# Optimization experiments

Measured on AMD Instinct MI355X. Metric: run time of the kernel, lower is better.

The kernel has to match this reference:

```python
import jax, jax.numpy as jnp
import numpy as np

N_NODES = 100000   # number of graph nodes
N_EDGES = 1000000  # number of edges
D_IN = 64          # input feature dim
D_OUT = 64         # output feature dim
N_RELS = 16        # number of relation types


def setup_inputs() -> dict:
    key = jax.random.key(0)
    k1, k2, k3, k4, k5 = jax.random.split(key, 5)
    feat = jax.random.normal(k1, (N_NODES, D_IN), dtype=jnp.float32)
    weight = jax.random.normal(k2, (N_RELS, D_IN, D_OUT), dtype=jnp.float32) * 0.05
    src = jax.random.randint(k3, (N_EDGES,), 0, N_NODES)
    dst = jax.random.randint(k4, (N_EDGES,), 0, N_NODES)
    etypes = jax.random.randint(k5, (N_EDGES,), 0, N_RELS)
    return {"feat": feat, "weight": weight, "src": src, "dst": dst, "etypes": etypes}


def reference(feat, weight, src, dst, etypes):
    # gather source-node features per edge: h = edges.src['h']
    h = feat[src]                                # [E, d_in]
    n_rels = weight.shape[0]
    e, d_out = h.shape[0], weight.shape[2]

    # gather_mm(h, weight, idx_b=etypes): m_e = h_e @ weight[etypes_e]
    # grouped-GEMM realized as R masked dense GEMMs (R is small, fixed);
    # avoids materializing the [E, d_in, d_out] gathered weight tensor.
    def step(m, rw):
        r, w_r = rw
        mask = jnp.where(etypes == r, 1.0, 0.0).astype(h.dtype)  # [E]
        m = m + mask[:, None] * (h @ w_r)                        # [E, d_out]
        return m, None

    m0 = jnp.zeros((e, d_out), dtype=h.dtype)
    m, _ = jax.lax.scan(step, m0, (jnp.arange(n_rels), weight))

    # update_all(..., fn.sum('m', 'h')): scatter-sum messages to dst nodes
    out = jax.ops.segment_sum(m, dst, num_segments=feat.shape[0])  # [N, d_out]
    return out
```

## Files before the change

### kernel.cpp

```cpp
#include <hip/hip_runtime.h>
#include <hip/hip_bf16.h>
#include <stdint.h>

#define NNODES 100000
#define NEDGES 1000000
#define DIM 64
#define NRELS 16
#define EPB 2048
#define NB ((NEDGES + EPB - 1) / EPB)
#define PADCAP (NEDGES + NRELS * 64)
#define MAXTILES (PADCAP / 64)
#define NDN NNODES
#define DCH 1024
#define NCHUNK ((NDN + DCH - 1) / DCH)

#define WS_NEED 151805824ull

using short8  = __attribute__((ext_vector_type(8))) short;
using floatx4 = __attribute__((ext_vector_type(4))) float;

__device__ __forceinline__ unsigned short f2bf(float f) {
    union { float f; uint32_t u; } v; v.f = f;
    uint32_t u = v.u;
    return (unsigned short)((u + 0x7FFFu + ((u >> 16) & 1u)) >> 16);
}
__device__ __forceinline__ float bf2f(uint32_t u16) {
    union { uint32_t u; float f; } v; v.u = u16 << 16;
    return v.f;
}
__device__ __forceinline__ uint32_t pk2(float a, float b) {
    __hip_bfloat162 h = __float22bfloat162_rn(make_float2(a, b));
    union { __hip_bfloat162 h; uint32_t u; } v; v.h = h;
    return v.u;
}

__global__ void k_convert_feat(const float* __restrict__ feat,
                               unsigned short* __restrict__ featB) {
    int i = (blockIdx.x * blockDim.x + threadIdx.x) * 4;
    const float4 f = *(const float4*)(feat + i);
    ushort4 o;
    o.x = f2bf(f.x); o.y = f2bf(f.y); o.z = f2bf(f.z); o.w = f2bf(f.w);
    *(ushort4*)(featB + i) = o;
}

__global__ void k_convert_w(const float* __restrict__ W,
                            unsigned short* __restrict__ Wt) {
    int t = blockIdx.x * blockDim.x + threadIdx.x;
    int r = t >> 12, n = (t >> 6) & 63, k = t & 63;
    Wt[t] = f2bf(W[(r << 12) + (k << 6) + n]);
}

__global__ void k_hist(const int* __restrict__ et, const int* __restrict__ dst,
                       int* __restrict__ hist, int* __restrict__ dhist,
                       unsigned short* __restrict__ rank) {
    __shared__ int cnt[16];
    if (threadIdx.x < 16) cnt[threadIdx.x] = 0;
    __syncthreads();
    int start = blockIdx.x * EPB;
    int end = min(NEDGES, start + EPB);
    for (int i = start + threadIdx.x; i < end; i += 256) {
        atomicAdd(&cnt[et[i]], 1);
        rank[i] = (unsigned short)atomicAdd(&dhist[dst[i]], 1);
    }
    __syncthreads();
    if (threadIdx.x < 16) hist[blockIdx.x * 16 + threadIdx.x] = cnt[threadIdx.x];
}

__global__ void k_scan(const int* __restrict__ hist, int* __restrict__ bbase,
                       int* __restrict__ Pve) {
    __shared__ int s_cnt[16];
    __shared__ int s_P[17];
    int w = threadIdx.x >> 6;
    int lane = threadIdx.x & 63;
    int carry = 0;
    for (int c = 0; c < NB; c += 64) {
        int idx = c + lane;
        int v = (idx < NB) ? hist[idx * 16 + w] : 0;
        int x = v;
        #pragma unroll
        for (int off = 1; off < 64; off <<= 1) {
            int y = __shfl_up(x, off);
            if (lane >= off) x += y;
        }
        if (idx < NB) bbase[idx * 16 + w] = carry + x - v;
        carry += __shfl(x, 63);
    }
    if (lane == 0) s_cnt[w] = carry;
    __syncthreads();
    if (threadIdx.x == 0) {
        int p = 0;
        for (int r = 0; r < 16; ++r) {
            s_P[r] = p;
            Pve[r] = p;
            Pve[17 + r] = p + s_cnt[r];
            p += (s_cnt[r] + 63) & ~63;
        }
        s_P[16] = p;
        Pve[16] = p;
    }
    __syncthreads();
    int pw = s_P[w];
    for (int idx = lane; idx < NB; idx += 64)
        bbase[idx * 16 + w] += pw;
}

__global__ void k_dscanA(const int* __restrict__ dhist, int* __restrict__ dbase,
                         int* __restrict__ csum) {
    __shared__ int wsum[16];
    __shared__ int woff[16];
    int t = threadIdx.x;
    int i = blockIdx.x * DCH + t;
    int v = (i < NDN) ? dhist[i] : 0;
    int lane = t & 63, wv = t >> 6;
    int x = v;
    #pragma unroll
    for (int off = 1; off < 64; off <<= 1) {
        int y = __shfl_up(x, off);
        if (lane >= off) x += y;
    }
    if (lane == 63) wsum[wv] = x;
    __syncthreads();
    if (wv == 0) {
        int s = (lane < 16) ? wsum[lane] : 0;
        #pragma unroll
        for (int off = 1; off < 16; off <<= 1) {
            int y = __shfl_up(s, off);
            if (lane >= off) s += y;
        }
        if (lane < 16) woff[lane] = s - wsum[lane];
        if (lane == 15) csum[blockIdx.x] = s;
    }
    __syncthreads();
    if (i < NDN) dbase[i] = woff[wv] + x - v;
}

__global__ void k_dscanB(int* __restrict__ dbase, const int* __restrict__ csum) {
    __shared__ int soff;
    int b = blockIdx.x, t = threadIdx.x;
    if (t < 64) {
        int s = ((t < b) ? csum[t] : 0) + ((t + 64 < b) ? csum[t + 64] : 0);
        #pragma unroll
        for (int off = 32; off >= 1; off >>= 1) s += __shfl_down(s, off);
        if (t == 0) soff = s;
    }
    __syncthreads();
    int i = b * DCH + t;
    if (i < NDN) dbase[i] += soff;
}

__global__ void k_scatter(const int* __restrict__ et, const int* __restrict__ src,
                          const int* __restrict__ dst, const int* __restrict__ bbase,
                          const int* __restrict__ dbase,
                          const unsigned short* __restrict__ rank,
                          int2* __restrict__ pairS, int buildPos) {
    __shared__ int base[16];
    if (threadIdx.x < 16) base[threadIdx.x] = bbase[blockIdx.x * 16 + threadIdx.x];
    __syncthreads();
    int start = blockIdx.x * EPB;
    int end = min(NEDGES, start + EPB);
    for (int i = start + threadIdx.x; i < end; i += 256) {
        int r = et[i];
        int pos = atomicAdd(&base[r], 1);
        int d = dst[i];
        int second = buildPos ? (dbase[d] + (int)rank[i]) : d;
        pairS[pos] = make_int2(src[i], second);
    }
}

__global__ void __launch_bounds__(256)
k_computeA(const unsigned short* __restrict__ featB,
           const unsigned short* __restrict__ Wt,
           const int2* __restrict__ pairS, const int* __restrict__ Pve,
           unsigned short* __restrict__ msgE) {
    __shared__ float lds[4][16 * 68];
    const int w = threadIdx.x >> 6;
    const int t = blockIdx.x * 4 + w;
    const int base = t * 64;
    const int total = Pve[16];
    if (base >= total) return;
    int r = 0;
    while (base >= Pve[r + 1]) ++r;
    const int validEnd = Pve[17 + r];
    const int lane = threadIdx.x & 63;
    const int quad = lane >> 4;
    const int l16 = lane & 15;

    const unsigned short* wr = Wt + (r << 12);
    short8 bfr[4][2];
    #pragma unroll
    for (int tn = 0; tn < 4; ++tn)
        #pragma unroll
        for (int ks = 0; ks < 2; ++ks)
            bfr[tn][ks] = *(const short8*)(wr + ((tn * 16 + l16) << 6) + ks * 32 + quad * 8);

    const int rr = lane >> 2, seg = lane & 3;
    #pragma unroll
    for (int tm = 0; tm < 4; ++tm) {
        int row = base + tm * 16 + l16;
        int s = (row < validEnd) ? pairS[row].x : 0;
        const unsigned short* fp = featB + (s << 6) + quad * 8;
        short8 a0 = *(const short8*)(fp);
        short8 a1 = *(const short8*)(fp + 32);
        #pragma unroll
        for (int tn = 0; tn < 4; ++tn) {
            floatx4 c = {0.f, 0.f, 0.f, 0.f};
            c = __builtin_amdgcn_mfma_f32_16x16x32_bf16(a0, bfr[tn][0], c, 0, 0, 0);
            c = __builtin_amdgcn_mfma_f32_16x16x32_bf16(a1, bfr[tn][1], c, 0, 0, 0);
            #pragma unroll
            for (int j = 0; j < 4; ++j)
                lds[w][(quad * 4 + j) * 68 + tn * 16 + l16] = c[j];
        }
        int rowi = base + tm * 16 + rr;
        int p = (rowi < validEnd) ? pairS[rowi].y : -1;
        if (p >= 0) {
            const float* lp = &lds[w][rr * 68 + seg * 16];
            uint4 o0, o1;
            o0.x = pk2(lp[0],  lp[1]);  o0.y = pk2(lp[2],  lp[3]);
            o0.z = pk2(lp[4],  lp[5]);  o0.w = pk2(lp[6],  lp[7]);
            o1.x = pk2(lp[8],  lp[9]);  o1.y = pk2(lp[10], lp[11]);
            o1.z = pk2(lp[12], lp[13]); o1.w = pk2(lp[14], lp[15]);
            uint32_t* op = (uint32_t*)(msgE + (size_t)p * 64 + seg * 16);
            *(uint4*)(op)     = o0;
            *(uint4*)(op + 4) = o1;
        }
    }
}

__global__ void __launch_bounds__(256)
k_reduce(const unsigned short* __restrict__ msgE,
         const int* __restrict__ dbase, float* __restrict__ out) {
    int n = blockIdx.x * 4 + (threadIdx.x >> 6);
    if (n >= NDN) return;
    int lane = threadIdx.x & 63;
    int start = dbase[n];
    int end = (n + 1 < NDN) ? dbase[n + 1] : NEDGES;
    int c4 = (lane & 15) * 4;
    float ax = 0.f, ay = 0.f, az = 0.f, aw = 0.f;
    for (int row = start + (lane >> 4); row < end; row += 4) {
        uint2 v = *(const uint2*)(msgE + (size_t)row * 64 + c4);
        ax += bf2f(v.x & 0xffffu); ay += bf2f(v.x >> 16);
        az += bf2f(v.y & 0xffffu); aw += bf2f(v.y >> 16);
    }
    ax += __shfl_xor(ax, 16); ax += __shfl_xor(ax, 32);
    ay += __shfl_xor(ay, 16); ay += __shfl_xor(ay, 32);
    az += __shfl_xor(az, 16); az += __shfl_xor(az, 32);
    aw += __shfl_xor(aw, 16); aw += __shfl_xor(aw, 32);
    if (lane < 16) {
        float4 o = make_float4(ax, ay, az, aw);
        *(float4*)(out + (size_t)n * 64 + lane * 4) = o;
    }
}

__global__ void __launch_bounds__(256)
k_compute(const unsigned short* __restrict__ featB,
          const unsigned short* __restrict__ Wt,
          const int2* __restrict__ pairS, const int* __restrict__ Pve,
          float* __restrict__ out) {
    const int t = blockIdx.x * 4 + (threadIdx.x >> 6);
    const int base = t * 64;
    const int total = Pve[16];
    if (base >= total) return;
    int r = 0;
    while (base >= Pve[r + 1]) ++r;
    const int validEnd = Pve[17 + r];
    const int lane = threadIdx.x & 63;
    const int quad = lane >> 4;
    const int l16 = lane & 15;

    const unsigned short* wr = Wt + (r << 12);
    short8 bfr[4][2];
    #pragma unroll
    for (int tn = 0; tn < 4; ++tn)
        #pragma unroll
        for (int ks = 0; ks < 2; ++ks)
            bfr[tn][ks] = *(const short8*)(wr + ((tn * 16 + l16) << 6) + ks * 32 + quad * 8);

    #pragma unroll
    for (int tm = 0; tm < 4; ++tm) {
        int row = base + tm * 16 + l16;
        int s = (row < validEnd) ? pairS[row].x : 0;
        const unsigned short* fp = featB + (s << 6) + quad * 8;
        short8 a0 = *(const short8*)(fp);
        short8 a1 = *(const short8*)(fp + 32);
        floatx4 cc[4];
        #pragma unroll
        for (int tn = 0; tn < 4; ++tn) {
            floatx4 c = {0.f, 0.f, 0.f, 0.f};
            c = __builtin_amdgcn_mfma_f32_16x16x32_bf16(a0, bfr[tn][0], c, 0, 0, 0);
            c = __builtin_amdgcn_mfma_f32_16x16x32_bf16(a1, bfr[tn][1], c, 0, 0, 0);
            cc[tn] = c;
        }
        int pos0 = base + tm * 16 + quad * 4;
        #pragma unroll
        for (int j = 0; j < 4; ++j) {
            if (pos0 + j < validEnd) {
                int dn = pairS[pos0 + j].y;
                float* op = out + (dn << 6) + l16;
                #pragma unroll
                for (int tn = 0; tn < 4; ++tn)
                    atomicAdd(op + tn * 16, cc[tn][j]);
            }
        }
    }
}

extern "C" void kernel_launch(void* const* d_in, const int* in_sizes, int n_in,
                              void* d_out, int out_size, void* d_ws, size_t ws_size,
                              hipStream_t stream) {
    const float* feat = (const float*)d_in[0];
    const float* W    = (const float*)d_in[1];
    const int* src    = (const int*)d_in[2];
    const int* dst    = (const int*)d_in[3];
    const int* et     = (const int*)d_in[4];
    float* out = (float*)d_out;
    char* ws = (char*)d_ws;

    unsigned short* featB = (unsigned short*)(ws);
    unsigned short* Wt    = (unsigned short*)(ws + 12800000);
    int* hist  = (int*)(ws + 12931072);
    int* bbase = (int*)(ws + 12963840);
    int* Pve   = (int*)(ws + 12996608);
    int* dhist = (int*)(ws + 12996864);
    int* dbase = (int*)(ws + 13396992);
    int* csum  = (int*)(ws + 13797120);
    unsigned short* rank = (unsigned short*)(ws + 13797632);
    int2* pairS = (int2*)(ws + 15797632);
    unsigned short* msgE = (unsigned short*)(ws + 23805824);

    const int usePhases = (ws_size >= WS_NEED) ? 1 : 0;

    k_convert_feat<<<6250, 256, 0, stream>>>(feat, featB);
    k_convert_w<<<256, 256, 0, stream>>>(W, Wt);
    hipMemsetAsync(dhist, 0, NDN * sizeof(int), stream);
    k_hist<<<NB, 256, 0, stream>>>(et, dst, hist, dhist, rank);
    k_scan<<<1, 1024, 0, stream>>>(hist, bbase, Pve);

    if (usePhases) {
        k_dscanA<<<NCHUNK, DCH, 0, stream>>>(dhist, dbase, csum);
        k_dscanB<<<NCHUNK, DCH, 0, stream>>>(dbase, csum);
        k_scatter<<<NB, 256, 0, stream>>>(et, src, dst, bbase, dbase, rank, pairS, 1);
        k_computeA<<<(MAXTILES + 3) / 4, 256, 0, stream>>>(featB, Wt, pairS, Pve, msgE);
        k_reduce<<<(NDN + 3) / 4, 256, 0, stream>>>(msgE, dbase, out);
    } else {
        hipMemsetAsync(d_out, 0, (size_t)out_size * sizeof(float), stream);
        k_scatter<<<NB, 256, 0, stream>>>(et, src, dst, bbase, dbase, rank, pairS, 0);
        k_compute<<<(MAXTILES + 3) / 4, 256, 0, stream>>>(featB, Wt, pairS, Pve, out);
    }
}
```

Before: 244.5 us.

## Fuse setup kernels, use nontemporal message stores, widen reduce loads

Merges the feature conversion, weight transpose/convert and histogram kernels into one launch that dispatches by block index, removing two kernel launches and their serialization gaps. The per-edge message writes in the compute kernel and the reads in the reduce kernel switch to nontemporal builtins to reduce cache pollution from the streaming bf16 message buffer. The reduce kernel now has each lane load 16 bytes (8 bf16) and processes 8 rows per wavefront iteration instead of 4, with an extra shuffle stage. Nontemporal hints may hurt if the message buffer would otherwise hit in L2 between compute and reduce.

```diff
diff --git a/kernel.cpp b/kernel.cpp
--- a/kernel.cpp
+++ b/kernel.cpp
@@ -14,10 +14,15 @@
 #define DCH 1024
 #define NCHUNK ((NDN + DCH - 1) / DCH)
 
+#define FEAT_BLKS 6250
+#define W_BLKS 256
+#define SETUP_BLKS (FEAT_BLKS + W_BLKS + NB)
+
 #define WS_NEED 151805824ull
 
 using short8  = __attribute__((ext_vector_type(8))) short;
 using floatx4 = __attribute__((ext_vector_type(4))) float;
+using uintx4  = __attribute__((ext_vector_type(4))) unsigned int;
 
 __device__ __forceinline__ unsigned short f2bf(float f) {
     union { float f; uint32_t u; } v; v.f = f;
@@ -34,36 +39,36 @@
     return v.u;
 }
 
-__global__ void k_convert_feat(const float* __restrict__ feat,
-                               unsigned short* __restrict__ featB) {
-    int i = (blockIdx.x * blockDim.x + threadIdx.x) * 4;
-    const float4 f = *(const float4*)(feat + i);
-    ushort4 o;
-    o.x = f2bf(f.x); o.y = f2bf(f.y); o.z = f2bf(f.z); o.w = f2bf(f.w);
-    *(ushort4*)(featB + i) = o;
-}
-
-__global__ void k_convert_w(const float* __restrict__ W,
-                            unsigned short* __restrict__ Wt) {
-    int t = blockIdx.x * blockDim.x + threadIdx.x;
-    int r = t >> 12, n = (t >> 6) & 63, k = t & 63;
-    Wt[t] = f2bf(W[(r << 12) + (k << 6) + n]);
-}
-
-__global__ void k_hist(const int* __restrict__ et, const int* __restrict__ dst,
-                       int* __restrict__ hist, int* __restrict__ dhist,
-                       unsigned short* __restrict__ rank) {
+__global__ void k_setup(const float* __restrict__ feat, const float* __restrict__ W,
+                        const int* __restrict__ et, const int* __restrict__ dst,
+                        unsigned short* __restrict__ featB, unsigned short* __restrict__ Wt,
+                        int* __restrict__ hist, int* __restrict__ dhist,
+                        unsigned short* __restrict__ rank) {
     __shared__ int cnt[16];
-    if (threadIdx.x < 16) cnt[threadIdx.x] = 0;
-    __syncthreads();
-    int start = blockIdx.x * EPB;
-    int end = min(NEDGES, start + EPB);
-    for (int i = start + threadIdx.x; i < end; i += 256) {
-        atomicAdd(&cnt[et[i]], 1);
-        rank[i] = (unsigned short)atomicAdd(&dhist[dst[i]], 1);
-    }
-    __syncthreads();
-    if (threadIdx.x < 16) hist[blockIdx.x * 16 + threadIdx.x] = cnt[threadIdx.x];
+    const int b = blockIdx.x;
+    if (b < FEAT_BLKS) {
+        int i = (b * 256 + threadIdx.x) * 4;
+        const float4 f = *(const float4*)(feat + i);
+        ushort4 o;
+        o.x = f2bf(f.x); o.y = f2bf(f.y); o.z = f2bf(f.z); o.w = f2bf(f.w);
+        *(ushort4*)(featB + i) = o;
+    } else if (b < FEAT_BLKS + W_BLKS) {
+        int t = (b - FEAT_BLKS) * 256 + threadIdx.x;
+        int r = t >> 12, n = (t >> 6) & 63, k = t & 63;
+        Wt[t] = f2bf(W[(r << 12) + (k << 6) + n]);
+    } else {
+        const int bb = b - (FEAT_BLKS + W_BLKS);
+        if (threadIdx.x < 16) cnt[threadIdx.x] = 0;
+        __syncthreads();
+        int start = bb * EPB;
+        int end = min(NEDGES, start + EPB);
+        for (int i = start + threadIdx.x; i < end; i += 256) {
+            atomicAdd(&cnt[et[i]], 1);
+            rank[i] = (unsigned short)atomicAdd(&dhist[dst[i]], 1);
+        }
+        __syncthreads();
+        if (threadIdx.x < 16) hist[bb * 16 + threadIdx.x] = cnt[threadIdx.x];
+    }
 }
 
 __global__ void k_scan(const int* __restrict__ hist, int* __restrict__ bbase,
@@ -214,14 +219,14 @@
         int p = (rowi < validEnd) ? pairS[rowi].y : -1;
         if (p >= 0) {
             const float* lp = &lds[w][rr * 68 + seg * 16];
-            uint4 o0, o1;
+            uintx4 o0, o1;
             o0.x = pk2(lp[0],  lp[1]);  o0.y = pk2(lp[2],  lp[3]);
             o0.z = pk2(lp[4],  lp[5]);  o0.w = pk2(lp[6],  lp[7]);
             o1.x = pk2(lp[8],  lp[9]);  o1.y = pk2(lp[10], lp[11]);
             o1.z = pk2(lp[12], lp[13]); o1.w = pk2(lp[14], lp[15]);
-            uint32_t* op = (uint32_t*)(msgE + (size_t)p * 64 + seg * 16);
-            *(uint4*)(op)     = o0;
-            *(uint4*)(op + 4) = o1;
+            uintx4* op = (uintx4*)(msgE + (size_t)p * 64 + seg * 16);
+            __builtin_nontemporal_store(o0, op);
+            __builtin_nontemporal_store(o1, op + 1);
         }
     }
 }
@@ -234,20 +239,28 @@
     int lane = threadIdx.x & 63;
     int start = dbase[n];
     int end = (n + 1 < NDN) ? dbase[n + 1] : NEDGES;
-    int c4 = (lane & 15) * 4;
-    float ax = 0.f, ay = 0.f, az = 0.f, aw = 0.f;
-    for (int row = start + (lane >> 4); row < end; row += 4) {
-        uint2 v = *(const uint2*)(msgE + (size_t)row * 64 + c4);
-        ax += bf2f(v.x & 0xffffu); ay += bf2f(v.x >> 16);
-        az += bf2f(v.y & 0xffffu); aw += bf2f(v.y >> 16);
-    }
-    ax += __shfl_xor(ax, 16); ax += __shfl_xor(ax, 32);
-    ay += __shfl_xor(ay, 16); ay += __shfl_xor(ay, 32);
-    az += __shfl_xor(az, 16); az += __shfl_xor(az, 32);
-    aw += __shfl_xor(aw, 16); aw += __shfl_xor(aw, 32);
-    if (lane < 16) {
-        float4 o = make_float4(ax, ay, az, aw);
-        *(float4*)(out + (size_t)n * 64 + lane * 4) = o;
+    int c8 = (lane & 7) * 8;
+    float a0 = 0.f, a1 = 0.f, a2 = 0.f, a3 = 0.f;
+    float a4 = 0.f, a5 = 0.f, a6 = 0.f, a7 = 0.f;
+    for (int row = start + (lane >> 3); row < end; row += 8) {
+        const uintx4* p = (const uintx4*)(msgE + (size_t)row * 64 + c8);
+        uintx4 v = __builtin_nontemporal_load(p);
+        a0 += bf2f(v.x & 0xffffu); a1 += bf2f(v.x >> 16);
+        a2 += bf2f(v.y & 0xffffu); a3 += bf2f(v.y >> 16);
+        a4 += bf2f(v.z & 0xffffu); a5 += bf2f(v.z >> 16);
+        a6 += bf2f(v.w & 0xffffu); a7 += bf2f(v.w >> 16);
+    }
+    #pragma unroll
+    for (int m = 8; m <= 32; m <<= 1) {
+        a0 += __shfl_xor(a0, m); a1 += __shfl_xor(a1, m);
+        a2 += __shfl_xor(a2, m); a3 += __shfl_xor(a3, m);
+        a4 += __shfl_xor(a4, m); a5 += __shfl_xor(a5, m);
+        a6 += __shfl_xor(a6, m); a7 += __shfl_xor(a7, m);
+    }
+    if (lane < 8) {
+        float* op = out + (size_t)n * 64 + lane * 8;
+        *(float4*)(op)     = make_float4(a0, a1, a2, a3);
+        *(float4*)(op + 4) = make_float4(a4, a5, a6, a7);
     }
 }
 
@@ -329,10 +342,8 @@
 
     const int usePhases = (ws_size >= WS_NEED) ? 1 : 0;
 
-    k_convert_feat<<<6250, 256, 0, stream>>>(feat, featB);
-    k_convert_w<<<256, 256, 0, stream>>>(W, Wt);
     hipMemsetAsync(dhist, 0, NDN * sizeof(int), stream);
-    k_hist<<<NB, 256, 0, stream>>>(et, dst, hist, dhist, rank);
+    k_setup<<<SETUP_BLKS, 256, 0, stream>>>(feat, W, et, dst, featB, Wt, hist, dhist, rank);
     k_scan<<<1, 1024, 0, stream>>>(hist, bbase, Pve);
 
     if (usePhases) {
```

Measured after the change: 256.8 us. 1.05x slower.
